# Optimization experiments

Hardware: AMD Instinct MI355X
Metric: run time of the kernel (lower is better)

The kernel has to match this reference:

```python
import jax, jax.numpy as jnp
import numpy as np

MAX_PATCH = 8   # max_patch_size: fixed span length
D_MODEL = 128
VOCAB = 256     # byte vocabulary
B, T = 16, 16384


def setup_inputs() -> dict:
    key = jax.random.key(0)
    k1, k2 = jax.random.split(key)
    x_u8 = jax.random.randint(k1, (B, T), 0, VOCAB, dtype=jnp.int32)
    byte_embed = jax.random.normal(k2, (VOCAB, D_MODEL), dtype=jnp.float32)
    return {"x_u8": x_u8, "byte_embed": byte_embed}


def reference(x_u8, byte_embed):
    # heuristic='fixed': spans are contiguous chunks of MAX_PATCH bytes.
    # Per span: embedding lookup then mean over the span -> [B, Tp, D].
    b, t = x_u8.shape
    tp = t // MAX_PATCH  # T divisible by MAX_PATCH (no ragged tail)
    emb = byte_embed[x_u8]  # gather: [B, T, D]
    out = emb.reshape(b, tp, MAX_PATCH, D_MODEL).mean(axis=2)  # [B, Tp, D]
    return out
```

## Files before the change

kernel.cpp:

```cpp
#include <hip/hip_runtime.h>
#include <hip/hip_bf16.h>


#define NPATCH  32768
#define TPB     1024
#define NBLK    256
#define NGROUPS ((NBLK * TPB) / 32)
#define ITERS   (NPATCH / NGROUPS)

__global__ __launch_bounds__(TPB, 1) void blt_patch_mean_lds(
    const int4* __restrict__ x4,
    const float4* __restrict__ emb4,
    float4* __restrict__ out4)
{
    extern __shared__ float4 tbl[];

    #pragma unroll
    for (int i = 0; i < 8; ++i) {
        int k = i * TPB + threadIdx.x;
        tbl[k] = emb4[k];
    }
    __syncthreads();

    const int group0 = ((int)blockIdx.x * TPB + (int)threadIdx.x) >> 5;
    const int col    = threadIdx.x & 31;

    #pragma unroll
    for (int it = 0; it < ITERS; ++it) {
        const int p = group0 + it * NGROUPS;

        int4 i0 = x4[p * 2];
        int4 i1 = x4[p * 2 + 1];

        float4 acc = make_float4(0.f, 0.f, 0.f, 0.f);
        #define ACCUM(r) { float4 v = tbl[(r) * 32 + col];                     \
                           acc.x += v.x; acc.y += v.y; acc.z += v.z; acc.w += v.w; }
        ACCUM(i0.x); ACCUM(i0.y); ACCUM(i0.z); ACCUM(i0.w);
        ACCUM(i1.x); ACCUM(i1.y); ACCUM(i1.z); ACCUM(i1.w);
        #undef ACCUM

        const float s = 0.125f;
        acc.x *= s; acc.y *= s; acc.z *= s; acc.w *= s;
        out4[p * 32 + col] = acc;
    }
}

extern "C" void kernel_launch(void* const* d_in, const int* in_sizes, int n_in,
                              void* d_out, int out_size, void* d_ws, size_t ws_size,
                              hipStream_t stream)
{
    const int4*   x4   = (const int4*)d_in[0];
    const float4* emb4 = (const float4*)d_in[1];
    float4*       out4 = (float4*)d_out;

    blt_patch_mean_lds<<<NBLK, TPB, 131072, stream>>>(x4, emb4, out4);
}
```

Baseline: 11.67 us.

## Load embedding table via async global-to-LDS DMA and overlap with first iteration

Replaces the register-staged copy of the embedding table into shared memory with asynchronous global_load_lds transfers and a static shared array. While the DMA is in flight, each thread computes its first patch by reading the embedding rows directly from global memory, then synchronises and runs the remaining iterations from LDS. This aims to hide the table-load latency behind useful work. It relies on the barrier waiting for the async LDS writes, and adds some extra global/L2 traffic for the first iteration.

```diff
diff --git a/kernel.cpp b/kernel.cpp
--- a/kernel.cpp
+++ b/kernel.cpp
@@ -5,7 +5,8 @@
 #define NPATCH  32768
 #define TPB     1024
 #define NBLK    256
-#define NGROUPS ((NBLK * TPB) / 32)
+#define GROUPS_PER_BLOCK (TPB / 32)
+#define NGROUPS (NBLK * GROUPS_PER_BLOCK)
 #define ITERS   (NPATCH / NGROUPS)
 
 __global__ __launch_bounds__(TPB, 1) void blt_patch_mean_lds(
@@ -13,33 +14,51 @@
     const float4* __restrict__ emb4,
     float4* __restrict__ out4)
 {
-    extern __shared__ float4 tbl[];
+    __shared__ float4 tbl[8192];
+
+    {
+        const float4* gsrc = emb4 + threadIdx.x;
+        float4*       ldst = tbl  + threadIdx.x;
+        #pragma unroll
+        for (int i = 0; i < 8; ++i) {
+            __builtin_amdgcn_global_load_lds(
+                (const __attribute__((address_space(1))) unsigned int*)(gsrc + i * TPB),
+                (__attribute__((address_space(3))) unsigned int*)(ldst + i * TPB),
+                16, 0, 0);
+        }
+    }
+
+    const int group0 = (int)blockIdx.x * GROUPS_PER_BLOCK + ((int)threadIdx.x >> 5);
+    const int col    = threadIdx.x & 31;
+    const float s    = 0.125f;
+
+    {
+        const int p = group0;
+        int4 i0 = x4[p * 2];
+        int4 i1 = x4[p * 2 + 1];
+        float4 acc = make_float4(0.f, 0.f, 0.f, 0.f);
+        #define ACCUMG(r) { float4 v = emb4[(r) * 32 + col];                   \
+                            acc.x += v.x; acc.y += v.y; acc.z += v.z; acc.w += v.w; }
+        ACCUMG(i0.x); ACCUMG(i0.y); ACCUMG(i0.z); ACCUMG(i0.w);
+        ACCUMG(i1.x); ACCUMG(i1.y); ACCUMG(i1.z); ACCUMG(i1.w);
+        #undef ACCUMG
+        acc.x *= s; acc.y *= s; acc.z *= s; acc.w *= s;
+        out4[p * 32 + col] = acc;
+    }
+
+    __syncthreads();
 
     #pragma unroll
-    for (int i = 0; i < 8; ++i) {
-        int k = i * TPB + threadIdx.x;
-        tbl[k] = emb4[k];
-    }
-    __syncthreads();
-
-    const int group0 = ((int)blockIdx.x * TPB + (int)threadIdx.x) >> 5;
-    const int col    = threadIdx.x & 31;
-
-    #pragma unroll
-    for (int it = 0; it < ITERS; ++it) {
+    for (int it = 1; it < ITERS; ++it) {
         const int p = group0 + it * NGROUPS;
-
         int4 i0 = x4[p * 2];
         int4 i1 = x4[p * 2 + 1];
-
         float4 acc = make_float4(0.f, 0.f, 0.f, 0.f);
         #define ACCUM(r) { float4 v = tbl[(r) * 32 + col];                     \
                            acc.x += v.x; acc.y += v.y; acc.z += v.z; acc.w += v.w; }
         ACCUM(i0.x); ACCUM(i0.y); ACCUM(i0.z); ACCUM(i0.w);
         ACCUM(i1.x); ACCUM(i1.y); ACCUM(i1.z); ACCUM(i1.w);
         #undef ACCUM
-
-        const float s = 0.125f;
         acc.x *= s; acc.y *= s; acc.z *= s; acc.w *= s;
         out4[p * 32 + col] = acc;
     }
@@ -53,5 +72,5 @@
     const float4* emb4 = (const float4*)d_in[1];
     float4*       out4 = (float4*)d_out;
 
-    blt_patch_mean_lds<<<NBLK, TPB, 131072, stream>>>(x4, emb4, out4);
+    blt_patch_mean_lds<<<NBLK, TPB, 0, stream>>>(x4, emb4, out4);
 }
```

Measured after the change: 12.55 us. +7.5%, slower.
